# Performance work log

Hardware: AMD Instinct MI355X
Metric: run time of the kernel (lower is better)

## Reference

```python
import jax, jax.numpy as jnp
import numpy as np

B, S, H, Q, K = 16, 4096, 1024, 1024, 2048


def setup_inputs() -> dict:
    key = jax.random.key(0)
    k0, k1, k2, k3, k4, k5 = jax.random.split(key, 6)
    return {
        "mask": jax.random.randint(k0, (B, 1, S), 0, 2, dtype=jnp.int32),
        "query": jax.random.normal(k1, (B, 1, Q), dtype=jnp.float32),
        "proj_key": jax.random.normal(k2, (B, S, H), dtype=jnp.float32),
        "value": jax.random.normal(k3, (B, S, K), dtype=jnp.float32),
        "Wq": jax.random.normal(k4, (H, Q), dtype=jnp.float32) * 0.02,
        "w_energy": jax.random.normal(k5, (H,), dtype=jnp.float32) * 0.02,
    }


def reference(mask, query, proj_key, value, Wq, w_energy):
    # query_layer: [B,1,Q] @ Wq^T -> [B,1,H]
    q = jnp.einsum("btq,hq->bth", query, Wq)
    # energy_layer(tanh(q + proj_key)): broadcast add over seq, dot with w_energy -> [B,S]
    scores = jnp.einsum("bsh,h->bs", jnp.tanh(q + proj_key), w_energy)
    scores = scores[:, None, :]  # [B,1,S]
    scores = jnp.where(mask == 0, -jnp.inf, scores)
    alphas = jax.nn.softmax(scores, axis=-1)  # [B,1,S]
    context = jnp.einsum("bts,bsk->btk", alphas, value)  # [B,1,K]
    return (context, alphas)
```

## Files before the change

kernel.cpp:

```cpp
#include <hip/hip_runtime.h>
#include <math.h>

#define B_ 16
#define S_ 4096
#define H_ 1024
#define Q_ 1024
#define K_ 2048

__device__ __forceinline__ float fast_tanh(float x) {
    float e = __expf(2.0f * x);
    float r = __builtin_amdgcn_rcpf(e + 1.0f);
    return 1.0f - 2.0f * r;
}

__device__ __forceinline__ float wave_reduce_sum(float v) {
#pragma unroll
    for (int off = 32; off > 0; off >>= 1)
        v += __shfl_xor(v, off, 64);
    return v;
}

__global__ __launch_bounds__(256) void qproj_kernel(const float* __restrict__ query,
                                                    const float* __restrict__ Wq,
                                                    float* __restrict__ qws) {
    int wave = (blockIdx.x * 256 + threadIdx.x) >> 6;
    int lane = threadIdx.x & 63;
    int b = wave >> 10;
    int h = wave & 1023;
    const float4* wrow = (const float4*)(Wq + (size_t)h * Q_);
    const float4* qrow = (const float4*)(query + (size_t)b * Q_);
    float acc = 0.f;
#pragma unroll
    for (int m = 0; m < 4; ++m) {
        int i = m * 64 + lane;
        float4 w = wrow[i];
        float4 q = qrow[i];
        acc += w.x * q.x + w.y * q.y + w.z * q.z + w.w * q.w;
    }
    acc = wave_reduce_sum(acc);
    if (lane == 0) qws[wave] = acc;
}

__global__ __launch_bounds__(256) void scores_kernel(const float* __restrict__ pk,
                                                     const float* __restrict__ qws,
                                                     const float* __restrict__ we,
                                                     const int* __restrict__ mask,
                                                     float* __restrict__ scores) {
    int row  = (blockIdx.x * 256 + threadIdx.x) >> 6;
    int lane = threadIdx.x & 63;
    if (mask[row] == 0) return;
    int b = row >> 12;
    const float4* prow = (const float4*)(pk + (size_t)row * H_);
    const float4* qrow = (const float4*)(qws + (size_t)b * H_);
    const float4* wrow = (const float4*)we;
    float acc = 0.f;
#pragma unroll
    for (int m = 0; m < 4; ++m) {
        int i = m * 64 + lane;
        float4 p = prow[i];
        float4 q = qrow[i];
        float4 w = wrow[i];
        acc += fast_tanh(q.x + p.x) * w.x;
        acc += fast_tanh(q.y + p.y) * w.y;
        acc += fast_tanh(q.z + p.z) * w.z;
        acc += fast_tanh(q.w + p.w) * w.w;
    }
    acc = wave_reduce_sum(acc);
    if (lane == 0) scores[row] = acc;
}

__global__ __launch_bounds__(256) void softmax_kernel(const float* __restrict__ scores,
                                                      const int* __restrict__ mask,
                                                      float* __restrict__ alphas,
                                                      int* __restrict__ cidx,
                                                      float* __restrict__ calpha,
                                                      int* __restrict__ count) {
    int b = blockIdx.x;
    int tid = threadIdx.x;
    __shared__ float red[8];
    __shared__ int scan[256];
    float v[16];
    int mk[16];
    int base = b * S_ + tid * 16;
    float lmax = -INFINITY;
    int myc = 0;
#pragma unroll
    for (int m = 0; m < 16; ++m) {
        float sc = scores[base + m];
        int mm = mask[base + m];
        mk[m] = mm;
        v[m] = mm ? sc : -INFINITY;
        lmax = fmaxf(lmax, v[m]);
        myc += (mm != 0);
    }
#pragma unroll
    for (int off = 32; off > 0; off >>= 1)
        lmax = fmaxf(lmax, __shfl_xor(lmax, off, 64));
    int wid = tid >> 6;
    if ((tid & 63) == 0) red[wid] = lmax;
    __syncthreads();
    float mx = fmaxf(fmaxf(red[0], red[1]), fmaxf(red[2], red[3]));
    float lsum = 0.f;
#pragma unroll
    for (int m = 0; m < 16; ++m) {
        float e = mk[m] ? __expf(v[m] - mx) : 0.f;
        v[m] = e;
        lsum += e;
    }
    lsum = wave_reduce_sum(lsum);
    if ((tid & 63) == 0) red[4 + wid] = lsum;
    __syncthreads();
    float total = red[4] + red[5] + red[6] + red[7];
    float rinv = 1.0f / total;
    scan[tid] = myc;
    __syncthreads();
    for (int off = 1; off < 256; off <<= 1) {
        int t = (tid >= off) ? scan[tid - off] : 0;
        __syncthreads();
        scan[tid] += t;
        __syncthreads();
    }
    int pos = scan[tid] - myc;
    if (tid == 255) count[b] = scan[255];
#pragma unroll
    for (int m = 0; m < 16; ++m) {
        float a = v[m] * rinv;
        alphas[base + m] = a;
        if (mk[m]) {
            cidx[b * S_ + pos]   = tid * 16 + m;
            calpha[b * S_ + pos] = a;
            pos++;
        }
    }
}

__global__ __launch_bounds__(256) void context_partial_kernel(const float* __restrict__ value,
                                                              const float* __restrict__ calpha,
                                                              const int* __restrict__ cidx,
                                                              const int* __restrict__ count,
                                                              float* __restrict__ partial,
                                                              int schunks, int Lmax) {
    extern __shared__ float sh[];
    float* la = sh;
    int*   li = (int*)(sh + Lmax);
    int c  = blockIdx.x;
    int kt = blockIdx.y;
    int b  = blockIdx.z;
    int tid = threadIdx.x;
    int cnt = count[b];
    int L = (cnt + schunks - 1) / schunks;
    int j0 = c * L;
    int j1 = j0 + L; if (j1 > cnt) j1 = cnt;
    int n = j1 - j0; if (n < 0) n = 0;
    for (int i = tid; i < n; i += 256) {
        la[i] = calpha[b * S_ + j0 + i];
        li[i] = cidx[b * S_ + j0 + i];
    }
    __syncthreads();
    const float* vbase = value + (size_t)b * S_ * K_ + kt * 1024;
    float4 acc = make_float4(0.f, 0.f, 0.f, 0.f);
#pragma unroll 4
    for (int i = 0; i < n; ++i) {
        float a = la[i];
        int   s = li[i];
        float4 vv = *((const float4*)(vbase + (size_t)s * K_) + tid);
        acc.x = fmaf(a, vv.x, acc.x);
        acc.y = fmaf(a, vv.y, acc.y);
        acc.z = fmaf(a, vv.z, acc.z);
        acc.w = fmaf(a, vv.w, acc.w);
    }
    float4* pout = (float4*)(partial + ((size_t)(b * schunks + c)) * K_ + kt * 1024) + tid;
    *pout = acc;
}

__global__ __launch_bounds__(256) void context_reduce_kernel(const float* __restrict__ partial,
                                                             float* __restrict__ ctx,
                                                             int schunks) {
    int idx = blockIdx.x * 256 + threadIdx.x;
    int b = idx >> 11;
    int k = idx & 2047;
    float acc = 0.f;
    for (int c = 0; c < schunks; ++c)
        acc += partial[((size_t)(b * schunks + c)) * K_ + k];
    ctx[idx] = acc;
}

extern "C" void kernel_launch(void* const* d_in, const int* in_sizes, int n_in,
                              void* d_out, int out_size, void* d_ws, size_t ws_size,
                              hipStream_t stream) {
    const int*   mask     = (const int*)d_in[0];
    const float* query    = (const float*)d_in[1];
    const float* proj_key = (const float*)d_in[2];
    const float* value    = (const float*)d_in[3];
    const float* Wq       = (const float*)d_in[4];
    const float* w_energy = (const float*)d_in[5];

    float* out    = (float*)d_out;
    float* ctx    = out;
    float* alphas = out + B_ * K_;

    float* ws      = (float*)d_ws;
    float* qws     = ws;
    float* scores  = qws + B_ * H_;
    float* calpha  = scores + B_ * S_;
    int*   cidx    = (int*)(calpha + B_ * S_);
    int*   count   = cidx + B_ * S_;
    float* partial = (float*)(count + 64);

    size_t used_head = (size_t)(B_ * H_ + 3 * B_ * S_ + 64);
    size_t avail = ws_size / 4;
    avail = (avail > used_head) ? (avail - used_head) : 0;
    int schunks = 32;
    while (schunks > 1 && (size_t)schunks * B_ * K_ > avail) schunks >>= 1;
    int Lmax = (S_ + schunks - 1) / schunks;

    qproj_kernel<<<(B_ * H_) / 4, 256, 0, stream>>>(query, Wq, qws);
    scores_kernel<<<(B_ * S_) / 4, 256, 0, stream>>>(proj_key, qws, w_energy, mask, scores);
    softmax_kernel<<<B_, 256, 0, stream>>>(scores, mask, alphas, cidx, calpha, count);
    dim3 g4(schunks, K_ / 1024, B_);
    size_t shbytes = (size_t)Lmax * (sizeof(float) + sizeof(int));
    context_partial_kernel<<<g4, 256, shbytes, stream>>>(value, calpha, cidx, count, partial,
                                                         schunks, Lmax);
    context_reduce_kernel<<<(B_ * K_) / 256, 256, 0, stream>>>(partial, ctx, schunks);
}
```

Before: 787.1 us.

## Batch rows per wave, nontemporal streaming loads, wider softmax and vectorized reduce

```diff
diff --git a/kernel.cpp b/kernel.cpp
--- a/kernel.cpp
+++ b/kernel.cpp
@@ -7,6 +7,8 @@
 #define Q_ 1024
 #define K_ 2048
 
+typedef float f4 __attribute__((ext_vector_type(4)));
+
 __device__ __forceinline__ float fast_tanh(float x) {
     float e = __expf(2.0f * x);
     float r = __builtin_amdgcn_rcpf(e + 1.0f);
@@ -23,22 +25,27 @@
 __global__ __launch_bounds__(256) void qproj_kernel(const float* __restrict__ query,
                                                     const float* __restrict__ Wq,
                                                     float* __restrict__ qws) {
-    int wave = (blockIdx.x * 256 + threadIdx.x) >> 6;
     int lane = threadIdx.x & 63;
-    int b = wave >> 10;
-    int h = wave & 1023;
-    const float4* wrow = (const float4*)(Wq + (size_t)h * Q_);
-    const float4* qrow = (const float4*)(query + (size_t)b * Q_);
-    float acc = 0.f;
-#pragma unroll
-    for (int m = 0; m < 4; ++m) {
-        int i = m * 64 + lane;
-        float4 w = wrow[i];
-        float4 q = qrow[i];
-        acc += w.x * q.x + w.y * q.y + w.z * q.z + w.w * q.w;
-    }
-    acc = wave_reduce_sum(acc);
-    if (lane == 0) qws[wave] = acc;
+    int wid  = threadIdx.x >> 6;
+    int gbase = blockIdx.x * 16;
+    int b = gbase >> 10;
+    const f4* qrow = (const f4*)(query + (size_t)b * Q_);
+    f4 qv[4];
+#pragma unroll
+    for (int m = 0; m < 4; ++m) qv[m] = qrow[m * 64 + lane];
+#pragma unroll
+    for (int t = 0; t < 4; ++t) {
+        int g = gbase + wid * 4 + t;
+        const f4* wrow = (const f4*)(Wq + (size_t)(g & 1023) * Q_);
+        float acc = 0.f;
+#pragma unroll
+        for (int m = 0; m < 4; ++m) {
+            f4 w = wrow[m * 64 + lane];
+            acc += w.x * qv[m].x + w.y * qv[m].y + w.z * qv[m].z + w.w * qv[m].w;
+        }
+        acc = wave_reduce_sum(acc);
+        if (lane == 0) qws[g] = acc;
+    }
 }
 
 __global__ __launch_bounds__(256) void scores_kernel(const float* __restrict__ pk,
@@ -46,92 +53,103 @@
                                                      const float* __restrict__ we,
                                                      const int* __restrict__ mask,
                                                      float* __restrict__ scores) {
-    int row  = (blockIdx.x * 256 + threadIdx.x) >> 6;
     int lane = threadIdx.x & 63;
-    if (mask[row] == 0) return;
-    int b = row >> 12;
-    const float4* prow = (const float4*)(pk + (size_t)row * H_);
-    const float4* qrow = (const float4*)(qws + (size_t)b * H_);
-    const float4* wrow = (const float4*)we;
-    float acc = 0.f;
+    int wid  = threadIdx.x >> 6;
+    int rowbase = blockIdx.x * 16;
+    int b = rowbase >> 12;
+    const f4* qrow = (const f4*)(qws + (size_t)b * H_);
+    const f4* wrow = (const f4*)we;
+    f4 qv[4], wv[4];
 #pragma unroll
     for (int m = 0; m < 4; ++m) {
-        int i = m * 64 + lane;
-        float4 p = prow[i];
-        float4 q = qrow[i];
-        float4 w = wrow[i];
-        acc += fast_tanh(q.x + p.x) * w.x;
-        acc += fast_tanh(q.y + p.y) * w.y;
-        acc += fast_tanh(q.z + p.z) * w.z;
-        acc += fast_tanh(q.w + p.w) * w.w;
-    }
-    acc = wave_reduce_sum(acc);
-    if (lane == 0) scores[row] = acc;
-}
-
-__global__ __launch_bounds__(256) void softmax_kernel(const float* __restrict__ scores,
-                                                      const int* __restrict__ mask,
-                                                      float* __restrict__ alphas,
-                                                      int* __restrict__ cidx,
-                                                      float* __restrict__ calpha,
-                                                      int* __restrict__ count) {
+        qv[m] = qrow[m * 64 + lane];
+        wv[m] = wrow[m * 64 + lane];
+    }
+    int mk[4];
+#pragma unroll
+    for (int t = 0; t < 4; ++t) mk[t] = mask[rowbase + wid * 4 + t];
+#pragma unroll
+    for (int t = 0; t < 4; ++t) {
+        if (mk[t] == 0) continue;
+        int row = rowbase + wid * 4 + t;
+        const f4* prow = (const f4*)(pk + (size_t)row * H_);
+        float acc = 0.f;
+#pragma unroll
+        for (int m = 0; m < 4; ++m) {
+            f4 p = __builtin_nontemporal_load(&prow[m * 64 + lane]);
+            f4 s = qv[m] + p;
+            acc += fast_tanh(s.x) * wv[m].x;
+            acc += fast_tanh(s.y) * wv[m].y;
+            acc += fast_tanh(s.z) * wv[m].z;
+            acc += fast_tanh(s.w) * wv[m].w;
+        }
+        acc = wave_reduce_sum(acc);
+        if (lane == 0) scores[row] = acc;
+    }
+}
+
+__global__ __launch_bounds__(1024) void softmax_kernel(const float* __restrict__ scores,
+                                                       const int* __restrict__ mask,
+                                                       float* __restrict__ alphas,
+                                                       int* __restrict__ cidx,
+                                                       float* __restrict__ calpha,
+                                                       int* __restrict__ count) {
     int b = blockIdx.x;
     int tid = threadIdx.x;
-    __shared__ float red[8];
-    __shared__ int scan[256];
-    float v[16];
-    int mk[16];
-    int base = b * S_ + tid * 16;
-    float lmax = -INFINITY;
-    int myc = 0;
-#pragma unroll
-    for (int m = 0; m < 16; ++m) {
-        float sc = scores[base + m];
-        int mm = mask[base + m];
-        mk[m] = mm;
-        v[m] = mm ? sc : -INFINITY;
-        lmax = fmaxf(lmax, v[m]);
-        myc += (mm != 0);
-    }
+    int lane = tid & 63;
+    int wid  = tid >> 6;
+    __shared__ float redmax[16];
+    __shared__ float redsum[16];
+    __shared__ int   wsum[16];
+    int base = b * S_ + tid * 4;
+    f4   sc = *(const f4*)(scores + base);
+    int4 mm = *(const int4*)(mask + base);
+    float v0 = mm.x ? sc.x : -INFINITY;
+    float v1 = mm.y ? sc.y : -INFINITY;
+    float v2 = mm.z ? sc.z : -INFINITY;
+    float v3 = mm.w ? sc.w : -INFINITY;
+    float lmax = fmaxf(fmaxf(v0, v1), fmaxf(v2, v3));
 #pragma unroll
     for (int off = 32; off > 0; off >>= 1)
         lmax = fmaxf(lmax, __shfl_xor(lmax, off, 64));
-    int wid = tid >> 6;
-    if ((tid & 63) == 0) red[wid] = lmax;
+    if (lane == 0) redmax[wid] = lmax;
     __syncthreads();
-    float mx = fmaxf(fmaxf(red[0], red[1]), fmaxf(red[2], red[3]));
-    float lsum = 0.f;
-#pragma unroll
-    for (int m = 0; m < 16; ++m) {
-        float e = mk[m] ? __expf(v[m] - mx) : 0.f;
-        v[m] = e;
-        lsum += e;
-    }
+    float mx = redmax[0];
+#pragma unroll
+    for (int w = 1; w < 16; ++w) mx = fmaxf(mx, redmax[w]);
+    float e0 = mm.x ? __expf(v0 - mx) : 0.f;
+    float e1 = mm.y ? __expf(v1 - mx) : 0.f;
+    float e2 = mm.z ? __expf(v2 - mx) : 0.f;
+    float e3 = mm.w ? __expf(v3 - mx) : 0.f;
+    float lsum = (e0 + e1) + (e2 + e3);
     lsum = wave_reduce_sum(lsum);
-    if ((tid & 63) == 0) red[4 + wid] = lsum;
+    if (lane == 0) redsum[wid] = lsum;
+    int myc = (mm.x != 0) + (mm.y != 0) + (mm.z != 0) + (mm.w != 0);
+    int x = myc;
+#pragma unroll
+    for (int off = 1; off < 64; off <<= 1) {
+        int y = __shfl_up(x, off, 64);
+        if (lane >= off) x += y;
+    }
+    if (lane == 63) wsum[wid] = x;
     __syncthreads();
-    float total = red[4] + red[5] + red[6] + red[7];
+    float total = 0.f;
+#pragma unroll
+    for (int w = 0; w < 16; ++w) total += redsum[w];
+    int woff = 0;
+    for (int w = 0; w < wid; ++w) woff += wsum[w];
+    int pos = woff + x - myc;
+    if (tid == 1023) count[b] = woff + x;
     float rinv = 1.0f / total;
-    scan[tid] = myc;
-    __syncthreads();
-    for (int off = 1; off < 256; off <<= 1) {
-        int t = (tid >= off) ? scan[tid - off] : 0;
-        __syncthreads();
-        scan[tid] += t;
-        __syncthreads();
-    }
-    int pos = scan[tid] - myc;
-    if (tid == 255) count[b] = scan[255];
-#pragma unroll
-    for (int m = 0; m < 16; ++m) {
-        float a = v[m] * rinv;
-        alphas[base + m] = a;
-        if (mk[m]) {
-            cidx[b * S_ + pos]   = tid * 16 + m;
-            calpha[b * S_ + pos] = a;
-            pos++;
-        }
-    }
+    float a0 = e0 * rinv, a1 = e1 * rinv, a2 = e2 * rinv, a3 = e3 * rinv;
+    f4 av; av.x = a0; av.y = a1; av.z = a2; av.w = a3;
+    *(f4*)(alphas + base) = av;
+    int sbase = b * S_;
+    int s0 = tid * 4;
+    if (mm.x) { cidx[sbase + pos] = s0 + 0; calpha[sbase + pos] = a0; pos++; }
+    if (mm.y) { cidx[sbase + pos] = s0 + 1; calpha[sbase + pos] = a1; pos++; }
+    if (mm.z) { cidx[sbase + pos] = s0 + 2; calpha[sbase + pos] = a2; pos++; }
+    if (mm.w) { cidx[sbase + pos] = s0 + 3; calpha[sbase + pos] = a3; pos++; }
 }
 
 __global__ __launch_bounds__(256) void context_partial_kernel(const float* __restrict__ value,
@@ -158,18 +176,18 @@
     }
     __syncthreads();
     const float* vbase = value + (size_t)b * S_ * K_ + kt * 1024;
-    float4 acc = make_float4(0.f, 0.f, 0.f, 0.f);
-#pragma unroll 4
+    f4 acc = {0.f, 0.f, 0.f, 0.f};
+#pragma unroll 8
     for (int i = 0; i < n; ++i) {
         float a = la[i];
         int   s = li[i];
-        float4 vv = *((const float4*)(vbase + (size_t)s * K_) + tid);
+        f4 vv = __builtin_nontemporal_load((const f4*)(vbase + (size_t)s * K_) + tid);
         acc.x = fmaf(a, vv.x, acc.x);
         acc.y = fmaf(a, vv.y, acc.y);
         acc.z = fmaf(a, vv.z, acc.z);
         acc.w = fmaf(a, vv.w, acc.w);
     }
-    float4* pout = (float4*)(partial + ((size_t)(b * schunks + c)) * K_ + kt * 1024) + tid;
+    f4* pout = (f4*)(partial + ((size_t)(b * schunks + c)) * K_ + kt * 1024) + tid;
     *pout = acc;
 }
 
@@ -177,12 +195,14 @@
                                                              float* __restrict__ ctx,
                                                              int schunks) {
     int idx = blockIdx.x * 256 + threadIdx.x;
-    int b = idx >> 11;
-    int k = idx & 2047;
-    float acc = 0.f;
-    for (int c = 0; c < schunks; ++c)
-        acc += partial[((size_t)(b * schunks + c)) * K_ + k];
-    ctx[idx] = acc;
+    int b  = idx >> 9;
+    int k4 = idx & 511;
+    f4 acc = {0.f, 0.f, 0.f, 0.f};
+    for (int c = 0; c < schunks; ++c) {
+        f4 p = *((const f4*)(partial + ((size_t)(b * schunks + c)) * K_) + k4);
+        acc.x += p.x; acc.y += p.y; acc.z += p.z; acc.w += p.w;
+    }
+    *((f4*)ctx + idx) = acc;
 }
 
 extern "C" void kernel_launch(void* const* d_in, const int* in_sizes, int n_in,
@@ -210,16 +230,16 @@
     size_t used_head = (size_t)(B_ * H_ + 3 * B_ * S_ + 64);
     size_t avail = ws_size / 4;
     avail = (avail > used_head) ? (avail - used_head) : 0;
-    int schunks = 32;
+    int schunks = 64;
     while (schunks > 1 && (size_t)schunks * B_ * K_ > avail) schunks >>= 1;
     int Lmax = (S_ + schunks - 1) / schunks;
 
-    qproj_kernel<<<(B_ * H_) / 4, 256, 0, stream>>>(query, Wq, qws);
-    scores_kernel<<<(B_ * S_) / 4, 256, 0, stream>>>(proj_key, qws, w_energy, mask, scores);
-    softmax_kernel<<<B_, 256, 0, stream>>>(scores, mask, alphas, cidx, calpha, count);
+    qproj_kernel<<<(B_ * H_) / 16, 256, 0, stream>>>(query, Wq, qws);
+    scores_kernel<<<(B_ * S_) / 16, 256, 0, stream>>>(proj_key, qws, w_energy, mask, scores);
+    softmax_kernel<<<B_, 1024, 0, stream>>>(scores, mask, alphas, cidx, calpha, count);
     dim3 g4(schunks, K_ / 1024, B_);
     size_t shbytes = (size_t)Lmax * (sizeof(float) + sizeof(int));
     context_partial_kernel<<<g4, 256, shbytes, stream>>>(value, calpha, cidx, count, partial,
                                                          schunks, Lmax);
-    context_reduce_kernel<<<(B_ * K_) / 256, 256, 0, stream>>>(partial, ctx, schunks);
-}
+    context_reduce_kernel<<<(B_ * K_) / 4 / 256, 256, 0, stream>>>(partial, ctx, schunks);
+}
```

New measurement: 764.7 us. 2.8% less time.
